# Kernel tuning notes

Measured on AMD Instinct MI355X. Metric: run time of the kernel, lower is better.

Reference implementation:

```python
import jax, jax.numpy as jnp
import numpy as np
import itertools

EPS = 1e-6
# Blade ordering for Cl(3,0): (), e1,e2,e3, e12,e13,e23, e123 -> grade of each blade
GRADE = np.array([0, 1, 1, 1, 2, 2, 2, 3])
_SL = [(0, 1), (1, 4), (4, 7), (7, 8)]  # blade slices per grade subspace


def build_cayley():
    """Geometric-product Cayley table for Cl(3,0) (Euclidean metric)."""
    blades = [()] + [c for r in range(1, 4) for c in itertools.combinations(range(3), r)]
    masks = [sum(1 << i for i in b) for b in blades]
    idx = {m: i for i, m in enumerate(masks)}
    C = np.zeros((8, 8, 8), np.float32)
    for i, a in enumerate(masks):
        for j, b in enumerate(masks):
            s, aa = 0, a >> 1
            while aa:
                s += bin(aa & b).count('1')
                aa >>= 1
            C[i, j, idx[a ^ b]] = -1.0 if (s & 1) else 1.0
    return C


def _qs(x):
    """Quadratic form per grade subspace: [..., 8] -> [..., 4] (Euclidean metric)."""
    x2 = x * x
    return jnp.concatenate([x2[..., a:b].sum(-1, keepdims=True) for a, b in _SL], axis=-1)


def _mvlinear(x, w, b=None):
    """Per-subspace multivector linear. x: [B, m, 8], w: [n, m, 4], b: [n] (scalar blade)."""
    out = jnp.einsum('bmi,nmi->bni', x, w[:, :, GRADE])
    if b is not None:
        out = out.at[..., 0].add(b)
    return out


def setup_inputs() -> dict:
    key = jax.random.key(0)
    ks = jax.random.split(key, 12)
    B, Fin, Fout = 131072, 16, 32
    return dict(
        x=jax.random.normal(ks[0], (B, Fin, 8), jnp.float32),
        w1=jax.random.normal(ks[1], (Fout, Fin, 4), jnp.float32) * float(1.0 / np.sqrt(Fin)),
        b1=jax.random.normal(ks[2], (Fout,), jnp.float32) * 0.1,
        a_relu=jax.random.uniform(ks[3], (Fout, 4), jnp.float32) + 0.5,
        b_relu=jax.random.normal(ks[4], (Fout, 4), jnp.float32) * 0.1,
        wl=jax.random.normal(ks[5], (Fout, Fout, 4), jnp.float32) * float(1.0 / np.sqrt(Fout)),
        bl=jax.random.normal(ks[6], (Fout,), jnp.float32) * 0.1,
        wr=jax.random.normal(ks[7], (Fout, Fout, 4), jnp.float32) * float(1.0 / np.sqrt(Fout)),
        a_norm=jax.random.normal(ks[8], (Fout, 4), jnp.float32) * 0.1,
        gp_w=jax.random.normal(ks[9], (Fout, 4, 4, 4), jnp.float32) * 0.5,
        a_ln=jax.random.uniform(ks[10], (Fout,), jnp.float32) + 0.5,
        cayley=jnp.asarray(build_cayley()),
    )


def reference(x, w1, b1, a_relu, b_relu, wl, bl, wr, a_norm, gp_w, a_ln, cayley):
    # --- MVLinear ---
    h = _mvlinear(x, w1, b1)  # [B, C, 8]
    # --- MVReLU: gate each channel by relu(a * invariants + b), invariants broadcast per grade ---
    inv = jnp.concatenate([h[..., :1], _qs(h)[..., 1:]], axis=-1)  # [B, C, 4]
    h = jax.nn.relu(a_relu * inv + b_relu)[..., GRADE] * h
    # --- SteerableGeometricProductLayer ---
    xr = _mvlinear(h, wr)  # linear_right (no bias)
    n = jnp.sqrt(jnp.abs(_qs(xr)))  # grade-wise norms
    n = jax.nn.sigmoid(a_norm) * (n - 1.0) + 1.0  # learned interpolation toward unit norm
    xr = xr / (n[..., GRADE] + EPS)
    # per-channel steerable geometric product weight: cayley * grade-block weight
    W = cayley[None] * gp_w[:, GRADE][:, :, GRADE][:, :, :, GRADE]  # [C, 8, 8, 8]
    h = (_mvlinear(h, wl, bl) + jnp.einsum('bci,cijk,bck->bcj', h, W, xr)) * float(1.0 / np.sqrt(2.0))
    # --- MVLayerNorm: divide by channel-mean multivector norm ---
    nrm = jnp.sqrt(_qs(h).sum(-1, keepdims=True)).mean(axis=1, keepdims=True) + EPS  # [B, 1, 1]
    return a_ln[:, None] * h / nrm
```

## Files before the change

kernel.cpp:

```cpp
#include <hip/hip_runtime.h>
#include <math.h>

#define EPSV 1e-6f

namespace {

constexpr int FIN   = 16;
constexpr int FOUT  = 32;
constexpr int SLOTS = 8;
constexpr int EPT   = 2;
constexpr int ELEMS = SLOTS * EPT;
constexpr int BLK   = 32 * SLOTS;
constexpr int GRID  = 1024;

constexpr int GJ[8][8] = {
  {0,1,2,3,4,5,6,7},
  {1,0,4,5,2,3,7,6},
  {2,4,0,6,1,7,3,5},
  {3,5,6,0,7,1,2,4},
  {4,2,1,7,0,6,5,3},
  {5,3,7,1,6,0,4,2},
  {6,7,3,2,5,4,0,1},
  {7,6,5,4,3,2,1,0},
};
constexpr float SREF[8][8] = {
  { 1, 1, 1, 1, 1, 1, 1, 1},
  { 1, 1, 1, 1, 1, 1, 1, 1},
  { 1,-1, 1, 1,-1,-1, 1,-1},
  { 1,-1,-1, 1, 1,-1,-1, 1},
  {-1, 1,-1,-1, 1, 1,-1, 1},
  {-1, 1, 1,-1,-1, 1, 1,-1},
  {-1,-1, 1,-1, 1,-1, 1, 1},
  {-1,-1, 1,-1, 1,-1, 1, 1},
};
constexpr int GSLOT[8][8] = {
  {0,1,1,1,2,2,2,3},
  {5,4,7,7,6,6,9,8},
  {5,7,4,7,6,9,6,8},
  {5,7,7,4,9,6,6,8},
  {13,11,11,15,10,14,14,12},
  {13,11,15,11,14,10,14,12},
  {13,15,11,11,14,14,10,12},
  {19,18,18,18,17,17,17,16},
};
constexpr int SLOT_OFF[20] = {0,5,10,15,17,20,22,25,27,30,34,37,39,40,42,45,51,54,57,60};

}

__global__ __launch_bounds__(BLK, 3)
void cge_block_kernel(const float* __restrict__ x,
                      const float* __restrict__ w1,
                      const float* __restrict__ b1,
                      const float* __restrict__ a_relu,
                      const float* __restrict__ b_relu,
                      const float* __restrict__ wl,
                      const float* __restrict__ bl,
                      const float* __restrict__ wr,
                      const float* __restrict__ a_norm,
                      const float* __restrict__ gp_w,
                      const float* __restrict__ a_ln,
                      float* __restrict__ out,
                      int B)
{
  __shared__ float4 w1s[FIN * FOUT];
  __shared__ float4 wrs[FOUT * FOUT];
  __shared__ float4 xs[2][ELEMS * FIN];
  __shared__ float4 hs[2][ELEMS * FOUT];

  const int tid  = threadIdx.x;
  const int c    = tid & 31;
  const int slot = tid >> 5;

  for (int idx = tid; idx < FIN * FOUT; idx += BLK) {
    int cc = idx >> 4, m = idx & 15;
    w1s[m * FOUT + cc] = ((const float4*)w1)[idx];
  }
  for (int idx = tid; idx < FOUT * FOUT; idx += BLK) {
    int cc = idx >> 5, m = idx & 31;
    wrs[m * FOUT + cc] = ((const float4*)wr)[idx];
  }

  float gw[20];
#pragma unroll
  for (int s = 0; s < 20; ++s) gw[s] = gp_w[c * 64 + SLOT_OFF[s]];
  const float  b1c  = b1[c];
  const float  blc  = bl[c];
  const float  alnc = a_ln[c];
  const float4 ar   = ((const float4*)a_relu)[c];
  const float4 br   = ((const float4*)b_relu)[c];
  const float4 an   = ((const float4*)a_norm)[c];
  const float  sg0  = 1.f / (1.f + expf(-an.x));
  const float  sg1  = 1.f / (1.f + expf(-an.y));
  const float  sg2  = 1.f / (1.f + expf(-an.z));
  const float  sg3  = 1.f / (1.f + expf(-an.w));
  const float4* wlc = ((const float4*)wl) + c * FOUT;

  const int ngroups = B / ELEMS;

  for (int g = blockIdx.x; g < ngroups; g += gridDim.x) {
    const int eb = g * ELEMS;
    __syncthreads();

    {
      const float4* xg = ((const float4*)x) + (size_t)eb * (FIN * 2);
#pragma unroll
      for (int t = 0; t < (ELEMS * FIN * 2) / BLK; ++t) {
        int idx = tid + t * BLK;
        float4 v = xg[idx];
        int e = idx >> 5, r = idx & 31;
        xs[r & 1][e * FIN + (r >> 1)] = v;
      }
    }
    __syncthreads();

    float h0[EPT][8];
#pragma unroll
    for (int e = 0; e < EPT; ++e) {
      h0[e][0] = b1c;
#pragma unroll
      for (int i = 1; i < 8; ++i) h0[e][i] = 0.f;
    }
#pragma unroll 4
    for (int m = 0; m < FIN; ++m) {
      const float4 w = w1s[m * FOUT + c];
#pragma unroll
      for (int e = 0; e < EPT; ++e) {
        const int le = slot * EPT + e;
        const float4 xlo = xs[0][le * FIN + m];
        const float4 xhi = xs[1][le * FIN + m];
        h0[e][0] += xlo.x * w.x;
        h0[e][1] += xlo.y * w.y;
        h0[e][2] += xlo.z * w.y;
        h0[e][3] += xlo.w * w.y;
        h0[e][4] += xhi.x * w.z;
        h0[e][5] += xhi.y * w.z;
        h0[e][6] += xhi.z * w.z;
        h0[e][7] += xhi.w * w.w;
      }
    }
#pragma unroll
    for (int e = 0; e < EPT; ++e) {
      const int le = slot * EPT + e;
      const float q1 = h0[e][1]*h0[e][1] + h0[e][2]*h0[e][2] + h0[e][3]*h0[e][3];
      const float q2 = h0[e][4]*h0[e][4] + h0[e][5]*h0[e][5] + h0[e][6]*h0[e][6];
      const float q3 = h0[e][7]*h0[e][7];
      const float g0 = fmaxf(ar.x * h0[e][0] + br.x, 0.f);
      const float g1 = fmaxf(ar.y * q1 + br.y, 0.f);
      const float g2 = fmaxf(ar.z * q2 + br.z, 0.f);
      const float g3 = fmaxf(ar.w * q3 + br.w, 0.f);
      h0[e][0] *= g0;
      h0[e][1] *= g1; h0[e][2] *= g1; h0[e][3] *= g1;
      h0[e][4] *= g2; h0[e][5] *= g2; h0[e][6] *= g2;
      h0[e][7] *= g3;
      hs[0][le * FOUT + c] = make_float4(h0[e][0], h0[e][1], h0[e][2], h0[e][3]);
      hs[1][le * FOUT + c] = make_float4(h0[e][4], h0[e][5], h0[e][6], h0[e][7]);
    }
    __syncthreads();

    float xr[EPT][8];
#pragma unroll
    for (int e = 0; e < EPT; ++e)
#pragma unroll
      for (int i = 0; i < 8; ++i) xr[e][i] = 0.f;
#pragma unroll 4
    for (int m = 0; m < FOUT; ++m) {
      const float4 w = wrs[m * FOUT + c];
#pragma unroll
      for (int e = 0; e < EPT; ++e) {
        const int le = slot * EPT + e;
        const float4 hlo = hs[0][le * FOUT + m];
        const float4 hhi = hs[1][le * FOUT + m];
        xr[e][0] += hlo.x * w.x;
        xr[e][1] += hlo.y * w.y;
        xr[e][2] += hlo.z * w.y;
        xr[e][3] += hlo.w * w.y;
        xr[e][4] += hhi.x * w.z;
        xr[e][5] += hhi.y * w.z;
        xr[e][6] += hhi.z * w.z;
        xr[e][7] += hhi.w * w.w;
      }
    }
#pragma unroll
    for (int e = 0; e < EPT; ++e) {
      const float q0 = xr[e][0]*xr[e][0];
      const float q1 = xr[e][1]*xr[e][1] + xr[e][2]*xr[e][2] + xr[e][3]*xr[e][3];
      const float q2 = xr[e][4]*xr[e][4] + xr[e][5]*xr[e][5] + xr[e][6]*xr[e][6];
      const float q3 = xr[e][7]*xr[e][7];
      const float r0 = 1.f / (sg0 * (sqrtf(q0) - 1.f) + 1.f + EPSV);
      const float r1 = 1.f / (sg1 * (sqrtf(q1) - 1.f) + 1.f + EPSV);
      const float r2 = 1.f / (sg2 * (sqrtf(q2) - 1.f) + 1.f + EPSV);
      const float r3 = 1.f / (sg3 * (sqrtf(q3) - 1.f) + 1.f + EPSV);
      xr[e][0] *= r0;
      xr[e][1] *= r1; xr[e][2] *= r1; xr[e][3] *= r1;
      xr[e][4] *= r2; xr[e][5] *= r2; xr[e][6] *= r2;
      xr[e][7] *= r3;
    }

    float h2[EPT][8];
#pragma unroll
    for (int e = 0; e < EPT; ++e) {
      h2[e][0] = blc;
#pragma unroll
      for (int i = 1; i < 8; ++i) h2[e][i] = 0.f;
    }
#pragma unroll 4
    for (int m = 0; m < FOUT; ++m) {
      const float4 w = wlc[m];
#pragma unroll
      for (int e = 0; e < EPT; ++e) {
        const int le = slot * EPT + e;
        const float4 hlo = hs[0][le * FOUT + m];
        const float4 hhi = hs[1][le * FOUT + m];
        h2[e][0] += hlo.x * w.x;
        h2[e][1] += hlo.y * w.y;
        h2[e][2] += hlo.z * w.y;
        h2[e][3] += hlo.w * w.y;
        h2[e][4] += hhi.x * w.z;
        h2[e][5] += hhi.y * w.z;
        h2[e][6] += hhi.z * w.z;
        h2[e][7] += hhi.w * w.w;
      }
    }
#pragma unroll
    for (int i = 0; i < 8; ++i) {
#pragma unroll
      for (int k = 0; k < 8; ++k) {
        const float w = SREF[i][k] * gw[GSLOT[i][k]];
#pragma unroll
        for (int e = 0; e < EPT; ++e) {
          h2[e][GJ[i][k]] += (w * h0[e][i]) * xr[e][k];
        }
      }
    }

#pragma unroll
    for (int e = 0; e < EPT; ++e) {
      const int le = slot * EPT + e;
      float s = 0.f;
#pragma unroll
      for (int i = 0; i < 8; ++i) {
        h2[e][i] *= 0.70710678118654752f;
        s += h2[e][i] * h2[e][i];
      }
      float n = sqrtf(s);
      n += __shfl_xor(n, 1);
      n += __shfl_xor(n, 2);
      n += __shfl_xor(n, 4);
      n += __shfl_xor(n, 8);
      n += __shfl_xor(n, 16);
      const float scale = alnc / (n * (1.f / FOUT) + EPSV);
      float4* o4 = (float4*)out + (size_t)(eb + le) * (FOUT * 2) + c * 2;
      o4[0] = make_float4(h2[e][0] * scale, h2[e][1] * scale,
                          h2[e][2] * scale, h2[e][3] * scale);
      o4[1] = make_float4(h2[e][4] * scale, h2[e][5] * scale,
                          h2[e][6] * scale, h2[e][7] * scale);
    }
  }
}

extern "C" void kernel_launch(void* const* d_in, const int* in_sizes, int n_in,
                              void* d_out, int out_size, void* d_ws, size_t ws_size,
                              hipStream_t stream) {
  const float* x      = (const float*)d_in[0];
  const float* w1     = (const float*)d_in[1];
  const float* b1     = (const float*)d_in[2];
  const float* a_relu = (const float*)d_in[3];
  const float* b_relu = (const float*)d_in[4];
  const float* wl     = (const float*)d_in[5];
  const float* bl     = (const float*)d_in[6];
  const float* wr     = (const float*)d_in[7];
  const float* a_norm = (const float*)d_in[8];
  const float* gp_w   = (const float*)d_in[9];
  const float* a_ln   = (const float*)d_in[10];

  const int B = in_sizes[0] / (FIN * 8);
  const int ngroups = B / ELEMS;
  const int grid = ngroups < GRID ? ngroups : GRID;

  cge_block_kernel<<<grid, BLK, 0, stream>>>(
      x, w1, b1, a_relu, b_relu, wl, bl, wr, a_norm, gp_w, a_ln,
      (float*)d_out, B);
}
```

Measured before the change: 407.3 us.

## Read x directly from global, fuse wr/wl matmul loops, raise occupancy

Drops the shared-memory staging of x and its two barriers per group; each thread now loads its elements' x values straight from global memory, which is uniform across the 32 channel lanes and so acts as a broadcast. The right and left linear projections are merged into one loop so each hs read is used by both accumulators. Launch bounds go from 3 to 4 blocks per SIMD, which lowers the register budget. The trade-offs are many redundant global loads of x served by the cache, and register pressure from holding xr and h2 together at the tighter occupancy target, which could cause spills.

```diff
diff --git a/kernel.cpp b/kernel.cpp
--- a/kernel.cpp
+++ b/kernel.cpp
@@ -7,10 +7,9 @@
 
 constexpr int FIN   = 16;
 constexpr int FOUT  = 32;
-constexpr int SLOTS = 8;
 constexpr int EPT   = 2;
-constexpr int ELEMS = SLOTS * EPT;
-constexpr int BLK   = 32 * SLOTS;
+constexpr int ELEMS = 8 * EPT;
+constexpr int BLK   = 256;
 constexpr int GRID  = 1024;
 
 constexpr int GJ[8][8] = {
@@ -47,7 +46,7 @@
 
 }
 
-__global__ __launch_bounds__(BLK, 3)
+__global__ __launch_bounds__(BLK, 4)
 void cge_block_kernel(const float* __restrict__ x,
                       const float* __restrict__ w1,
                       const float* __restrict__ b1,
@@ -64,7 +63,6 @@
 {
   __shared__ float4 w1s[FIN * FOUT];
   __shared__ float4 wrs[FOUT * FOUT];
-  __shared__ float4 xs[2][ELEMS * FIN];
   __shared__ float4 hs[2][ELEMS * FOUT];
 
   const int tid  = threadIdx.x;
@@ -96,22 +94,12 @@
   const float4* wlc = ((const float4*)wl) + c * FOUT;
 
   const int ngroups = B / ELEMS;
+  const float4* xg = (const float4*)x;
+
+  __syncthreads();
 
   for (int g = blockIdx.x; g < ngroups; g += gridDim.x) {
     const int eb = g * ELEMS;
-    __syncthreads();
-
-    {
-      const float4* xg = ((const float4*)x) + (size_t)eb * (FIN * 2);
-#pragma unroll
-      for (int t = 0; t < (ELEMS * FIN * 2) / BLK; ++t) {
-        int idx = tid + t * BLK;
-        float4 v = xg[idx];
-        int e = idx >> 5, r = idx & 31;
-        xs[r & 1][e * FIN + (r >> 1)] = v;
-      }
-    }
-    __syncthreads();
 
     float h0[EPT][8];
 #pragma unroll
@@ -126,8 +114,9 @@
 #pragma unroll
       for (int e = 0; e < EPT; ++e) {
         const int le = slot * EPT + e;
-        const float4 xlo = xs[0][le * FIN + m];
-        const float4 xhi = xs[1][le * FIN + m];
+        const size_t base = (size_t)(eb + le) * (FIN * 2) + m * 2;
+        const float4 xlo = xg[base];
+        const float4 xhi = xg[base + 1];
         h0[e][0] += xlo.x * w.x;
         h0[e][1] += xlo.y * w.y;
         h0[e][2] += xlo.z * w.y;
@@ -138,6 +127,9 @@
         h0[e][7] += xhi.w * w.w;
       }
     }
+
+    __syncthreads();
+
 #pragma unroll
     for (int e = 0; e < EPT; ++e) {
       const int le = slot * EPT + e;
@@ -158,28 +150,43 @@
     __syncthreads();
 
     float xr[EPT][8];
-#pragma unroll
-    for (int e = 0; e < EPT; ++e)
+    float h2[EPT][8];
+#pragma unroll
+    for (int e = 0; e < EPT; ++e) {
+      h2[e][0] = blc;
+#pragma unroll
+      for (int i = 1; i < 8; ++i) h2[e][i] = 0.f;
 #pragma unroll
       for (int i = 0; i < 8; ++i) xr[e][i] = 0.f;
+    }
 #pragma unroll 4
     for (int m = 0; m < FOUT; ++m) {
-      const float4 w = wrs[m * FOUT + c];
+      const float4 wrv = wrs[m * FOUT + c];
+      const float4 wlv = wlc[m];
 #pragma unroll
       for (int e = 0; e < EPT; ++e) {
         const int le = slot * EPT + e;
         const float4 hlo = hs[0][le * FOUT + m];
         const float4 hhi = hs[1][le * FOUT + m];
-        xr[e][0] += hlo.x * w.x;
-        xr[e][1] += hlo.y * w.y;
-        xr[e][2] += hlo.z * w.y;
-        xr[e][3] += hlo.w * w.y;
-        xr[e][4] += hhi.x * w.z;
-        xr[e][5] += hhi.y * w.z;
-        xr[e][6] += hhi.z * w.z;
-        xr[e][7] += hhi.w * w.w;
-      }
-    }
+        xr[e][0] += hlo.x * wrv.x;
+        xr[e][1] += hlo.y * wrv.y;
+        xr[e][2] += hlo.z * wrv.y;
+        xr[e][3] += hlo.w * wrv.y;
+        xr[e][4] += hhi.x * wrv.z;
+        xr[e][5] += hhi.y * wrv.z;
+        xr[e][6] += hhi.z * wrv.z;
+        xr[e][7] += hhi.w * wrv.w;
+        h2[e][0] += hlo.x * wlv.x;
+        h2[e][1] += hlo.y * wlv.y;
+        h2[e][2] += hlo.z * wlv.y;
+        h2[e][3] += hlo.w * wlv.y;
+        h2[e][4] += hhi.x * wlv.z;
+        h2[e][5] += hhi.y * wlv.z;
+        h2[e][6] += hhi.z * wlv.z;
+        h2[e][7] += hhi.w * wlv.w;
+      }
+    }
+
 #pragma unroll
     for (int e = 0; e < EPT; ++e) {
       const float q0 = xr[e][0]*xr[e][0];
@@ -196,31 +203,6 @@
       xr[e][7] *= r3;
     }
 
-    float h2[EPT][8];
-#pragma unroll
-    for (int e = 0; e < EPT; ++e) {
-      h2[e][0] = blc;
-#pragma unroll
-      for (int i = 1; i < 8; ++i) h2[e][i] = 0.f;
-    }
-#pragma unroll 4
-    for (int m = 0; m < FOUT; ++m) {
-      const float4 w = wlc[m];
-#pragma unroll
-      for (int e = 0; e < EPT; ++e) {
-        const int le = slot * EPT + e;
-        const float4 hlo = hs[0][le * FOUT + m];
-        const float4 hhi = hs[1][le * FOUT + m];
-        h2[e][0] += hlo.x * w.x;
-        h2[e][1] += hlo.y * w.y;
-        h2[e][2] += hlo.z * w.y;
-        h2[e][3] += hlo.w * w.y;
-        h2[e][4] += hhi.x * w.z;
-        h2[e][5] += hhi.y * w.z;
-        h2[e][6] += hhi.z * w.z;
-        h2[e][7] += hhi.w * w.w;
-      }
-    }
 #pragma unroll
     for (int i = 0; i < 8; ++i) {
 #pragma unroll
```

After: 442.9 us. +8.7%, slower.
